# Optimization experiments

Measured on AMD Instinct MI355X. Metric: run time of the kernel, lower is better.

Reference implementation:

```python
import jax, jax.numpy as jnp
import numpy as np

B, D_IN, D_H = 262144, 64, 128


def setup_inputs() -> dict:
    key = jax.random.key(0)
    ks = jax.random.split(key, 15)
    mk = lambda k, shape: jax.random.normal(k, shape, dtype=jnp.float32) * 0.05
    return {
        "x": mk(ks[0], (B, D_IN)),
        "prev_hidden": mk(ks[1], (B, D_H)),
        "prev_memory": mk(ks[2], (B, D_H)),
        "Wi_w": mk(ks[3], (D_H, D_IN)), "Wi_b": mk(ks[4], (D_H,)),
        "Vi_w": mk(ks[5], (D_H, D_H)),  "Vi_b": mk(ks[6], (D_H,)),
        "Wf_w": mk(ks[7], (D_H, D_IN)), "Wf_b": mk(ks[8], (D_H,)),
        "Vf_w": mk(ks[9], (D_H, D_H)),  "Vf_b": mk(ks[10], (D_H,)),
        "Wo_w": mk(ks[11], (D_H, D_IN)), "Wo_b": mk(ks[12], (D_H,)),
        "Vo_w": mk(ks[13], (D_H, D_H)),  "Vo_b": mk(ks[14], (D_H,)),
    }


def _lin(x, w, b):
    # nn.Linear: x @ w.T + b
    return jnp.einsum('bi,oi->bo', x, w) + b


def reference(x, prev_hidden, prev_memory,
              Wi_w, Wi_b, Vi_w, Vi_b,
              Wf_w, Wf_b, Vf_w, Vf_b,
              Wo_w, Wo_b, Vo_w, Vo_b):
    sig = jax.nn.sigmoid
    wi_x = _lin(x, Wi_w, Wi_b)  # reused for both I and C (quirk of source)
    I = sig(wi_x + _lin(prev_hidden, Vi_w, Vi_b))
    F = sig(_lin(x, Wf_w, Wf_b) + _lin(prev_hidden, Vf_w, Vf_b))
    O = sig(_lin(x, Wo_w, Wo_b) + _lin(prev_hidden, Vo_w, Vo_b))
    # source uses Wi/Vi (not Wc/Vc) and sigmoid for the candidate, on F*prev_hidden
    C = sig(wi_x + _lin(F * prev_hidden, Vi_w, Vi_b))
    Ct = F * prev_memory + I * C
    current_hidden = O * jnp.tanh(Ct)
    return (Ct, current_hidden)
```

## Files before the change

### kernel.cpp

```cpp
#include <hip/hip_runtime.h>
#include <hip/hip_bf16.h>

typedef __bf16 bf8 __attribute__((ext_vector_type(8)));
typedef float  f4  __attribute__((ext_vector_type(4)));

#define RT 64
#define MS 4

__device__ __forceinline__ float fsig(float v) {
    return __builtin_amdgcn_rcpf(1.0f + __expf(-v));
}

__device__ __forceinline__ bf8 cvt8(f4 a, f4 b) {
    bf8 r;
    r[0] = (__bf16)a[0]; r[1] = (__bf16)a[1]; r[2] = (__bf16)a[2]; r[3] = (__bf16)a[3];
    r[4] = (__bf16)b[0]; r[5] = (__bf16)b[1]; r[6] = (__bf16)b[2]; r[7] = (__bf16)b[3];
    return r;
}

__device__ __forceinline__ unsigned pk2(float a, float b) {
    union { __bf16 h; unsigned short s; } ua, ub;
    ua.h = (__bf16)a; ub.h = (__bf16)b;
    return ((unsigned)ub.s << 16) | (unsigned)ua.s;
}
__device__ __forceinline__ float upk(unsigned v, int hi) {
    union { unsigned short s; __bf16 h; } u;
    u.s = (unsigned short)(hi ? (v >> 16) : (v & 0xffffu));
    return (float)u.h;
}

__global__ void pack_weights(
    const float* __restrict__ Wi, const float* __restrict__ Vi,
    const float* __restrict__ Wf, const float* __restrict__ Vf,
    const float* __restrict__ Wo, const float* __restrict__ Vo,
    const float* __restrict__ Wib, const float* __restrict__ Vib,
    const float* __restrict__ Wfb, const float* __restrict__ Vfb,
    const float* __restrict__ Wob, const float* __restrict__ Vob,
    __bf16* __restrict__ wsW, float* __restrict__ wsB)
{
    const int t = blockIdx.x * 256 + threadIdx.x;
    if (t < 73728) {
        const int fg   = t >> 9;
        const int l8   = t & 511;
        const int lane = l8 >> 3, j = l8 & 7;
        const int w    = fg / 18, f = fg % 18;
        const int nrow = w * 16 + (lane & 15);
        const int kq   = (lane >> 4) << 3;
        float v;
        if (f < 6) {
            const float* M = (f < 2) ? Wi : (f < 4) ? Wf : Wo;
            v = M[nrow * 64 + (f & 1) * 32 + kq + j];
        } else {
            const int f2 = f - 6;
            const float* M = (f2 < 4) ? Vi : (f2 < 8) ? Vf : Vo;
            v = M[nrow * 128 + (f2 & 3) * 32 + kq + j];
        }
        wsW[t] = (__bf16)v;
    } else if (t < 74112) {
        const int c = t - 73728;
        const int col = c & 127, m = c >> 7;
        wsB[c] = (m == 0) ? Wib[col] + Vib[col]
               : (m == 1) ? Wfb[col] + Vfb[col]
                          : Wob[col] + Vob[col];
    }
}

__global__ __launch_bounds__(512, 2) void lstm_main(
    const float* __restrict__ x, const float* __restrict__ h,
    const float* __restrict__ mem,
    const bf8* __restrict__ wsW, const float* __restrict__ wsB,
    float* __restrict__ out, long long Bn)
{
    __shared__ __align__(16) __bf16 smX[RT * 64];
    __shared__ __align__(16) __bf16 smH[RT * 128];
    __shared__ __align__(16) __bf16 smG[RT * 128 + 64];

    const int tid  = threadIdx.x;
    const int lane = tid & 63;
    const int wv   = tid >> 6;
    const int nrow = wv * 16 + (lane & 15);
    const int kq   = (lane >> 4) << 3;
    const long long b0 = (long long)blockIdx.x * RT;

    const bf8* wbase = wsW + (size_t)wv * 18 * 64 + lane;

    {
        const int rowx = tid >> 3, kbx = tid & 7;
        const float* px = x + (size_t)(b0 + rowx) * 64 + kbx * 8;
        *(bf8*)&smX[rowx * 64 + ((kbx * 8) ^ ((rowx & 7) << 3))] =
            cvt8(*(const f4*)px, *(const f4*)(px + 4));
#pragma unroll
        for (int ph = 0; ph < 2; ++ph) {
            const int task = tid + ph * 512;
            const int rowh = task >> 4, kbh = task & 15;
            const float* q = h + (size_t)(b0 + rowh) * 128 + kbh * 8;
            *(bf8*)&smH[rowh * 128 + ((kbh * 8) ^ ((rowh & 7) << 3))] =
                cvt8(*(const f4*)q, *(const f4*)(q + 4));
        }
    }

    bf8 Wf0 = wbase[2 * 64],  Wf1 = wbase[3 * 64];
    bf8 Vf0 = wbase[10 * 64], Vf1 = wbase[11 * 64];
    bf8 Vf2 = wbase[12 * 64], Vf3 = wbase[13 * 64];
    const float bF = wsB[128 + nrow];
    __syncthreads();

    f4 memv[MS];
#pragma unroll
    for (int ms = 0; ms < MS; ++ms) {
#pragma unroll
        for (int i = 0; i < 4; ++i) {
            const int row = ms * 16 + ((lane >> 4) << 2) + i;
            memv[ms][i] = mem[(size_t)(b0 + row) * 128 + nrow];
        }
    }

    unsigned FP[MS][2];
#pragma unroll
    for (int ms = 0; ms < MS; ++ms) {
        const int rA = ms * 16 + (lane & 15);
        f4 pf = {0.f, 0.f, 0.f, 0.f};
        {
            bf8 a0 = *(const bf8*)&smX[rA * 64 + ((0 * 32 + kq) ^ ((rA & 7) << 3))];
            bf8 a1 = *(const bf8*)&smX[rA * 64 + ((1 * 32 + kq) ^ ((rA & 7) << 3))];
            pf = __builtin_amdgcn_mfma_f32_16x16x32_bf16(a0, Wf0, pf, 0, 0, 0);
            pf = __builtin_amdgcn_mfma_f32_16x16x32_bf16(a1, Wf1, pf, 0, 0, 0);
        }
        {
            bf8 a0 = *(const bf8*)&smH[rA * 128 + ((0 * 32 + kq) ^ ((rA & 7) << 3))];
            bf8 a1 = *(const bf8*)&smH[rA * 128 + ((1 * 32 + kq) ^ ((rA & 7) << 3))];
            bf8 a2 = *(const bf8*)&smH[rA * 128 + ((2 * 32 + kq) ^ ((rA & 7) << 3))];
            bf8 a3 = *(const bf8*)&smH[rA * 128 + ((3 * 32 + kq) ^ ((rA & 7) << 3))];
            pf = __builtin_amdgcn_mfma_f32_16x16x32_bf16(a0, Vf0, pf, 0, 0, 0);
            pf = __builtin_amdgcn_mfma_f32_16x16x32_bf16(a1, Vf1, pf, 0, 0, 0);
            pf = __builtin_amdgcn_mfma_f32_16x16x32_bf16(a2, Vf2, pf, 0, 0, 0);
            pf = __builtin_amdgcn_mfma_f32_16x16x32_bf16(a3, Vf3, pf, 0, 0, 0);
        }
        float fv[4];
#pragma unroll
        for (int i = 0; i < 4; ++i) {
            const float Fi  = fsig(pf[i] + bF);
            const int   row = ms * 16 + ((lane >> 4) << 2) + i;
            const int   e   = row * 128 + (nrow ^ ((row & 7) << 3));
            smG[e] = (__bf16)(Fi * (float)smH[e]);
            fv[i]  = Fi;
        }
        FP[ms][0] = pk2(fv[0], fv[1]);
        FP[ms][1] = pk2(fv[2], fv[3]);
    }
    __syncthreads();
    __builtin_amdgcn_sched_barrier(0);

    bf8 Wi0 = wbase[0],      Wi1 = wbase[64];
    bf8 Vi0 = wbase[6 * 64], Vi1 = wbase[7 * 64];
    bf8 Vi2 = wbase[8 * 64], Vi3 = wbase[9 * 64];
    const float bI = wsB[nrow];
    const size_t outH = (size_t)Bn * 128;

    f4 ThS[MS];
#pragma unroll
    for (int ms = 0; ms < MS; ++ms) {
        const int rA = ms * 16 + (lane & 15);
        f4 wix = {0.f, 0.f, 0.f, 0.f};
        {
            bf8 a0 = *(const bf8*)&smX[rA * 64 + ((0 * 32 + kq) ^ ((rA & 7) << 3))];
            bf8 a1 = *(const bf8*)&smX[rA * 64 + ((1 * 32 + kq) ^ ((rA & 7) << 3))];
            wix = __builtin_amdgcn_mfma_f32_16x16x32_bf16(a0, Wi0, wix, 0, 0, 0);
            wix = __builtin_amdgcn_mfma_f32_16x16x32_bf16(a1, Wi1, wix, 0, 0, 0);
        }
        f4 aI = wix, aC = wix;
        {
            bf8 a0 = *(const bf8*)&smH[rA * 128 + ((0 * 32 + kq) ^ ((rA & 7) << 3))];
            bf8 a1 = *(const bf8*)&smH[rA * 128 + ((1 * 32 + kq) ^ ((rA & 7) << 3))];
            bf8 a2 = *(const bf8*)&smH[rA * 128 + ((2 * 32 + kq) ^ ((rA & 7) << 3))];
            bf8 a3 = *(const bf8*)&smH[rA * 128 + ((3 * 32 + kq) ^ ((rA & 7) << 3))];
            aI = __builtin_amdgcn_mfma_f32_16x16x32_bf16(a0, Vi0, aI, 0, 0, 0);
            aI = __builtin_amdgcn_mfma_f32_16x16x32_bf16(a1, Vi1, aI, 0, 0, 0);
            aI = __builtin_amdgcn_mfma_f32_16x16x32_bf16(a2, Vi2, aI, 0, 0, 0);
            aI = __builtin_amdgcn_mfma_f32_16x16x32_bf16(a3, Vi3, aI, 0, 0, 0);
        }
        {
            bf8 g0 = *(const bf8*)&smG[rA * 128 + ((0 * 32 + kq) ^ ((rA & 7) << 3))];
            bf8 g1 = *(const bf8*)&smG[rA * 128 + ((1 * 32 + kq) ^ ((rA & 7) << 3))];
            bf8 g2 = *(const bf8*)&smG[rA * 128 + ((2 * 32 + kq) ^ ((rA & 7) << 3))];
            bf8 g3 = *(const bf8*)&smG[rA * 128 + ((3 * 32 + kq) ^ ((rA & 7) << 3))];
            aC = __builtin_amdgcn_mfma_f32_16x16x32_bf16(g0, Vi0, aC, 0, 0, 0);
            aC = __builtin_amdgcn_mfma_f32_16x16x32_bf16(g1, Vi1, aC, 0, 0, 0);
            aC = __builtin_amdgcn_mfma_f32_16x16x32_bf16(g2, Vi2, aC, 0, 0, 0);
            aC = __builtin_amdgcn_mfma_f32_16x16x32_bf16(g3, Vi3, aC, 0, 0, 0);
        }
#pragma unroll
        for (int i = 0; i < 4; ++i) {
            const float Iv = fsig(aI[i] + bI);
            const float Cv = fsig(aC[i] + bI);
            const float Fi = upk(FP[ms][i >> 1], i & 1);
            const float ct = Fi * memv[ms][i] + Iv * Cv;
            const float e2 = __expf(2.0f * ct);
            ThS[ms][i] = 1.0f - 2.0f * __builtin_amdgcn_rcpf(e2 + 1.0f);
            const int   row = ms * 16 + ((lane >> 4) << 2) + i;
            const size_t g  = (size_t)(b0 + row) * 128 + nrow;
            out[g] = ct;
        }
    }
    __builtin_amdgcn_sched_barrier(0);

    bf8 Wo0 = wbase[4 * 64],  Wo1 = wbase[5 * 64];
    bf8 Vo0 = wbase[14 * 64], Vo1 = wbase[15 * 64];
    bf8 Vo2 = wbase[16 * 64], Vo3 = wbase[17 * 64];
    const float bO = wsB[256 + nrow];
#pragma unroll
    for (int ms = 0; ms < MS; ++ms) {
        const int rA = ms * 16 + (lane & 15);
        f4 po = {0.f, 0.f, 0.f, 0.f};
        {
            bf8 a0 = *(const bf8*)&smX[rA * 64 + ((0 * 32 + kq) ^ ((rA & 7) << 3))];
            bf8 a1 = *(const bf8*)&smX[rA * 64 + ((1 * 32 + kq) ^ ((rA & 7) << 3))];
            po = __builtin_amdgcn_mfma_f32_16x16x32_bf16(a0, Wo0, po, 0, 0, 0);
            po = __builtin_amdgcn_mfma_f32_16x16x32_bf16(a1, Wo1, po, 0, 0, 0);
        }
        {
            bf8 a0 = *(const bf8*)&smH[rA * 128 + ((0 * 32 + kq) ^ ((rA & 7) << 3))];
            bf8 a1 = *(const bf8*)&smH[rA * 128 + ((1 * 32 + kq) ^ ((rA & 7) << 3))];
            bf8 a2 = *(const bf8*)&smH[rA * 128 + ((2 * 32 + kq) ^ ((rA & 7) << 3))];
            bf8 a3 = *(const bf8*)&smH[rA * 128 + ((3 * 32 + kq) ^ ((rA & 7) << 3))];
            po = __builtin_amdgcn_mfma_f32_16x16x32_bf16(a0, Vo0, po, 0, 0, 0);
            po = __builtin_amdgcn_mfma_f32_16x16x32_bf16(a1, Vo1, po, 0, 0, 0);
            po = __builtin_amdgcn_mfma_f32_16x16x32_bf16(a2, Vo2, po, 0, 0, 0);
            po = __builtin_amdgcn_mfma_f32_16x16x32_bf16(a3, Vo3, po, 0, 0, 0);
        }
#pragma unroll
        for (int i = 0; i < 4; ++i) {
            const float Ov = fsig(po[i] + bO);
            const int   row = ms * 16 + ((lane >> 4) << 2) + i;
            const size_t g  = (size_t)(b0 + row) * 128 + nrow;
            out[outH + g] = Ov * ThS[ms][i];
        }
    }
}

extern "C" void kernel_launch(void* const* d_in, const int* in_sizes, int n_in,
                              void* d_out, int out_size, void* d_ws, size_t ws_size,
                              hipStream_t stream) {
    const float* x   = (const float*)d_in[0];
    const float* h   = (const float*)d_in[1];
    const float* mem = (const float*)d_in[2];
    const float* Wi  = (const float*)d_in[3];
    const float* Wib = (const float*)d_in[4];
    const float* Vi  = (const float*)d_in[5];
    const float* Vib = (const float*)d_in[6];
    const float* Wf  = (const float*)d_in[7];
    const float* Wfb = (const float*)d_in[8];
    const float* Vf  = (const float*)d_in[9];
    const float* Vfb = (const float*)d_in[10];
    const float* Wo  = (const float*)d_in[11];
    const float* Wob = (const float*)d_in[12];
    const float* Vo  = (const float*)d_in[13];
    const float* Vob = (const float*)d_in[14];
    float* out = (float*)d_out;

    __bf16* wsW = (__bf16*)d_ws;
    float*  wsB = (float*)((char*)d_ws + 147456);

    pack_weights<<<290, 256, 0, stream>>>(Wi, Vi, Wf, Vf, Wo, Vo,
                                          Wib, Vib, Wfb, Vfb, Wob, Vob, wsW, wsB);

    const long long Bn = (long long)(in_sizes[1] / 128);
    const int blocks = (int)(Bn / RT);

    lstm_main<<<blocks, 512, 0, stream>>>(x, h, mem, (const bf8*)wsW, wsB, out, Bn);
}
```

Baseline: 160.0 us.

## Double row tile per block, stream memory loads, pack tanh to bf16

Each block now handles 128 rows instead of 64, so per-wave weight fragment loads are amortized over twice as many rows, and the grid is half as large. The up-front load of all prev_memory values into registers is replaced by a rolling three-slot prefetch issued two sub-tiles ahead, and the tanh results held for the output-gate pass are packed to bf16 pairs. Both register changes offset the pressure from the larger tile. LDS use roughly doubles, which may stop two blocks fitting per CU, and storing tanh in bf16 lowers the precision of the hidden-state output.

```diff
diff --git a/kernel.cpp b/kernel.cpp
--- a/kernel.cpp
+++ b/kernel.cpp
@@ -4,8 +4,8 @@
 typedef __bf16 bf8 __attribute__((ext_vector_type(8)));
 typedef float  f4  __attribute__((ext_vector_type(4)));
 
-#define RT 64
-#define MS 4
+#define RT 128
+#define MS 8
 
 __device__ __forceinline__ float fsig(float v) {
     return __builtin_amdgcn_rcpf(1.0f + __expf(-v));
@@ -73,7 +73,7 @@
 {
     __shared__ __align__(16) __bf16 smX[RT * 64];
     __shared__ __align__(16) __bf16 smH[RT * 128];
-    __shared__ __align__(16) __bf16 smG[RT * 128 + 64];
+    __shared__ __align__(16) __bf16 smG[RT * 128];
 
     const int tid  = threadIdx.x;
     const int lane = tid & 63;
@@ -85,12 +85,16 @@
     const bf8* wbase = wsW + (size_t)wv * 18 * 64 + lane;
 
     {
-        const int rowx = tid >> 3, kbx = tid & 7;
-        const float* px = x + (size_t)(b0 + rowx) * 64 + kbx * 8;
-        *(bf8*)&smX[rowx * 64 + ((kbx * 8) ^ ((rowx & 7) << 3))] =
-            cvt8(*(const f4*)px, *(const f4*)(px + 4));
 #pragma unroll
         for (int ph = 0; ph < 2; ++ph) {
+            const int task = tid + ph * 512;
+            const int rowx = task >> 3, kbx = task & 7;
+            const float* px = x + (size_t)(b0 + rowx) * 64 + kbx * 8;
+            *(bf8*)&smX[rowx * 64 + ((kbx * 8) ^ ((rowx & 7) << 3))] =
+                cvt8(*(const f4*)px, *(const f4*)(px + 4));
+        }
+#pragma unroll
+        for (int ph = 0; ph < 4; ++ph) {
             const int task = tid + ph * 512;
             const int rowh = task >> 4, kbh = task & 15;
             const float* q = h + (size_t)(b0 + rowh) * 128 + kbh * 8;
@@ -104,16 +108,6 @@
     bf8 Vf2 = wbase[12 * 64], Vf3 = wbase[13 * 64];
     const float bF = wsB[128 + nrow];
     __syncthreads();
-
-    f4 memv[MS];
-#pragma unroll
-    for (int ms = 0; ms < MS; ++ms) {
-#pragma unroll
-        for (int i = 0; i < 4; ++i) {
-            const int row = ms * 16 + ((lane >> 4) << 2) + i;
-            memv[ms][i] = mem[(size_t)(b0 + row) * 128 + nrow];
-        }
-    }
 
     unsigned FP[MS][2];
 #pragma unroll
@@ -157,9 +151,23 @@
     const float bI = wsB[nrow];
     const size_t outH = (size_t)Bn * 128;
 
-    f4 ThS[MS];
+    auto ldmem = [&](int ms) -> f4 {
+        f4 r;
+#pragma unroll
+        for (int i = 0; i < 4; ++i) {
+            const int row = ms * 16 + ((lane >> 4) << 2) + i;
+            r[i] = mem[(size_t)(b0 + row) * 128 + nrow];
+        }
+        return r;
+    };
+    f4 mv[3];
+    mv[0] = ldmem(0);
+    mv[1] = ldmem(1);
+
+    unsigned ThP[MS][2];
 #pragma unroll
     for (int ms = 0; ms < MS; ++ms) {
+        if (ms + 2 < MS) mv[(ms + 2) % 3] = ldmem(ms + 2);
         const int rA = ms * 16 + (lane & 15);
         f4 wix = {0.f, 0.f, 0.f, 0.f};
         {
@@ -189,18 +197,21 @@
             aC = __builtin_amdgcn_mfma_f32_16x16x32_bf16(g2, Vi2, aC, 0, 0, 0);
             aC = __builtin_amdgcn_mfma_f32_16x16x32_bf16(g3, Vi3, aC, 0, 0, 0);
         }
+        float th[4];
 #pragma unroll
         for (int i = 0; i < 4; ++i) {
             const float Iv = fsig(aI[i] + bI);
             const float Cv = fsig(aC[i] + bI);
             const float Fi = upk(FP[ms][i >> 1], i & 1);
-            const float ct = Fi * memv[ms][i] + Iv * Cv;
+            const float ct = Fi * mv[ms % 3][i] + Iv * Cv;
             const float e2 = __expf(2.0f * ct);
-            ThS[ms][i] = 1.0f - 2.0f * __builtin_amdgcn_rcpf(e2 + 1.0f);
+            th[i] = 1.0f - 2.0f * __builtin_amdgcn_rcpf(e2 + 1.0f);
             const int   row = ms * 16 + ((lane >> 4) << 2) + i;
             const size_t g  = (size_t)(b0 + row) * 128 + nrow;
             out[g] = ct;
         }
+        ThP[ms][0] = pk2(th[0], th[1]);
+        ThP[ms][1] = pk2(th[2], th[3]);
     }
     __builtin_amdgcn_sched_barrier(0);
 
@@ -231,9 +242,10 @@
 #pragma unroll
         for (int i = 0; i < 4; ++i) {
             const float Ov = fsig(po[i] + bO);
+            const float th = upk(ThP[ms][i >> 1], i & 1);
             const int   row = ms * 16 + ((lane >> 4) << 2) + i;
             const size_t g  = (size_t)(b0 + row) * 128 + nrow;
-            out[outH + g] = Ov * ThS[ms][i];
+            out[outH + g] = Ov * th;
         }
     }
 }
```

Result: no change. 158.0 us (-1.2%).

## Make blocks persistent over 8 row tiles with double-buffered x/h prefetch

Applied to the files above, without the earlier changes.

Each block now processes 8 consecutive 64-row tiles instead of one. The x and h loads for the next tile are issued into registers during the current tile's gate computation and written into a second shared-memory buffer at the end of the iteration. The intent is to hide global load latency behind MFMA work and to amortize block launch and bias setup. The tanh values are kept packed as bf16 to limit register pressure. In exchange the grid shrinks 8x, to 512 blocks, which may underfill the CUs, and shared-memory use rises, which can lower occupancy.

```diff
diff --git a/kernel.cpp b/kernel.cpp
--- a/kernel.cpp
+++ b/kernel.cpp
@@ -4,8 +4,9 @@
 typedef __bf16 bf8 __attribute__((ext_vector_type(8)));
 typedef float  f4  __attribute__((ext_vector_type(4)));
 
-#define RT 64
-#define MS 4
+#define RT    64
+#define MS    4
+#define TILES 8
 
 __device__ __forceinline__ float fsig(float v) {
     return __builtin_amdgcn_rcpf(1.0f + __expf(-v));
@@ -71,169 +72,209 @@
     const bf8* __restrict__ wsW, const float* __restrict__ wsB,
     float* __restrict__ out, long long Bn)
 {
-    __shared__ __align__(16) __bf16 smX[RT * 64];
-    __shared__ __align__(16) __bf16 smH[RT * 128];
-    __shared__ __align__(16) __bf16 smG[RT * 128 + 64];
+    __shared__ __align__(16) __bf16 smX[2][RT * 64];
+    __shared__ __align__(16) __bf16 smH[2][RT * 128];
+    __shared__ __align__(16) __bf16 smG[RT * 128];
 
     const int tid  = threadIdx.x;
     const int lane = tid & 63;
     const int wv   = tid >> 6;
     const int nrow = wv * 16 + (lane & 15);
     const int kq   = (lane >> 4) << 3;
-    const long long b0 = (long long)blockIdx.x * RT;
+    const long long tile0 = (long long)blockIdx.x * TILES;
+    const size_t outH = (size_t)Bn * 128;
 
     const bf8* wbase = wsW + (size_t)wv * 18 * 64 + lane;
+    const float bI = wsB[nrow];
+    const float bF = wsB[128 + nrow];
+    const float bO = wsB[256 + nrow];
+
+    const int rowx  = tid >> 3,  kbx  = tid & 7;
+    const int xoff  = rowx * 64 + ((kbx * 8) ^ ((rowx & 7) << 3));
+    const int rowh0 = tid >> 4,  kbh  = tid & 15;
+    const int hoff0 = rowh0 * 128 + ((kbh * 8) ^ ((rowh0 & 7) << 3));
+    const int rowh1 = rowh0 + 32;
+    const int hoff1 = rowh1 * 128 + ((kbh * 8) ^ ((rowh1 & 7) << 3));
 
     {
-        const int rowx = tid >> 3, kbx = tid & 7;
-        const float* px = x + (size_t)(b0 + rowx) * 64 + kbx * 8;
-        *(bf8*)&smX[rowx * 64 + ((kbx * 8) ^ ((rowx & 7) << 3))] =
-            cvt8(*(const f4*)px, *(const f4*)(px + 4));
-#pragma unroll
-        for (int ph = 0; ph < 2; ++ph) {
-            const int task = tid + ph * 512;
-            const int rowh = task >> 4, kbh = task & 15;
-            const float* q = h + (size_t)(b0 + rowh) * 128 + kbh * 8;
-            *(bf8*)&smH[rowh * 128 + ((kbh * 8) ^ ((rowh & 7) << 3))] =
-                cvt8(*(const f4*)q, *(const f4*)(q + 4));
-        }
+        const long long b0s = tile0 * RT;
+        const float* px  = x + (size_t)(b0s + rowx) * 64 + kbx * 8;
+        f4 xa = *(const f4*)px,  xb = *(const f4*)(px + 4);
+        const float* ph0 = h + (size_t)(b0s + rowh0) * 128 + kbh * 8;
+        f4 ha = *(const f4*)ph0, hb = *(const f4*)(ph0 + 4);
+        const float* ph1 = h + (size_t)(b0s + rowh1) * 128 + kbh * 8;
+        f4 hc = *(const f4*)ph1, hd = *(const f4*)(ph1 + 4);
+        *(bf8*)&smX[0][xoff]  = cvt8(xa, xb);
+        *(bf8*)&smH[0][hoff0] = cvt8(ha, hb);
+        *(bf8*)&smH[0][hoff1] = cvt8(hc, hd);
     }
 
-    bf8 Wf0 = wbase[2 * 64],  Wf1 = wbase[3 * 64];
-    bf8 Vf0 = wbase[10 * 64], Vf1 = wbase[11 * 64];
-    bf8 Vf2 = wbase[12 * 64], Vf3 = wbase[13 * 64];
-    const float bF = wsB[128 + nrow];
-    __syncthreads();
-
-    f4 memv[MS];
-#pragma unroll
-    for (int ms = 0; ms < MS; ++ms) {
-#pragma unroll
-        for (int i = 0; i < 4; ++i) {
-            const int row = ms * 16 + ((lane >> 4) << 2) + i;
-            memv[ms][i] = mem[(size_t)(b0 + row) * 128 + nrow];
-        }
-    }
-
-    unsigned FP[MS][2];
-#pragma unroll
-    for (int ms = 0; ms < MS; ++ms) {
-        const int rA = ms * 16 + (lane & 15);
-        f4 pf = {0.f, 0.f, 0.f, 0.f};
-        {
-            bf8 a0 = *(const bf8*)&smX[rA * 64 + ((0 * 32 + kq) ^ ((rA & 7) << 3))];
-            bf8 a1 = *(const bf8*)&smX[rA * 64 + ((1 * 32 + kq) ^ ((rA & 7) << 3))];
-            pf = __builtin_amdgcn_mfma_f32_16x16x32_bf16(a0, Wf0, pf, 0, 0, 0);
-            pf = __builtin_amdgcn_mfma_f32_16x16x32_bf16(a1, Wf1, pf, 0, 0, 0);
-        }
-        {
-            bf8 a0 = *(const bf8*)&smH[rA * 128 + ((0 * 32 + kq) ^ ((rA & 7) << 3))];
-            bf8 a1 = *(const bf8*)&smH[rA * 128 + ((1 * 32 + kq) ^ ((rA & 7) << 3))];
-            bf8 a2 = *(const bf8*)&smH[rA * 128 + ((2 * 32 + kq) ^ ((rA & 7) << 3))];
-            bf8 a3 = *(const bf8*)&smH[rA * 128 + ((3 * 32 + kq) ^ ((rA & 7) << 3))];
-            pf = __builtin_amdgcn_mfma_f32_16x16x32_bf16(a0, Vf0, pf, 0, 0, 0);
-            pf = __builtin_amdgcn_mfma_f32_16x16x32_bf16(a1, Vf1, pf, 0, 0, 0);
-            pf = __builtin_amdgcn_mfma_f32_16x16x32_bf16(a2, Vf2, pf, 0, 0, 0);
-            pf = __builtin_amdgcn_mfma_f32_16x16x32_bf16(a3, Vf3, pf, 0, 0, 0);
-        }
-        float fv[4];
-#pragma unroll
-        for (int i = 0; i < 4; ++i) {
-            const float Fi  = fsig(pf[i] + bF);
-            const int   row = ms * 16 + ((lane >> 4) << 2) + i;
-            const int   e   = row * 128 + (nrow ^ ((row & 7) << 3));
-            smG[e] = (__bf16)(Fi * (float)smH[e]);
-            fv[i]  = Fi;
-        }
-        FP[ms][0] = pk2(fv[0], fv[1]);
-        FP[ms][1] = pk2(fv[2], fv[3]);
-    }
-    __syncthreads();
-    __builtin_amdgcn_sched_barrier(0);
-
-    bf8 Wi0 = wbase[0],      Wi1 = wbase[64];
-    bf8 Vi0 = wbase[6 * 64], Vi1 = wbase[7 * 64];
-    bf8 Vi2 = wbase[8 * 64], Vi3 = wbase[9 * 64];
-    const float bI = wsB[nrow];
-    const size_t outH = (size_t)Bn * 128;
-
-    f4 ThS[MS];
-#pragma unroll
-    for (int ms = 0; ms < MS; ++ms) {
-        const int rA = ms * 16 + (lane & 15);
-        f4 wix = {0.f, 0.f, 0.f, 0.f};
-        {
-            bf8 a0 = *(const bf8*)&smX[rA * 64 + ((0 * 32 + kq) ^ ((rA & 7) << 3))];
-            bf8 a1 = *(const bf8*)&smX[rA * 64 + ((1 * 32 + kq) ^ ((rA & 7) << 3))];
-            wix = __builtin_amdgcn_mfma_f32_16x16x32_bf16(a0, Wi0, wix, 0, 0, 0);
-            wix = __builtin_amdgcn_mfma_f32_16x16x32_bf16(a1, Wi1, wix, 0, 0, 0);
-        }
-        f4 aI = wix, aC = wix;
-        {
-            bf8 a0 = *(const bf8*)&smH[rA * 128 + ((0 * 32 + kq) ^ ((rA & 7) << 3))];
-            bf8 a1 = *(const bf8*)&smH[rA * 128 + ((1 * 32 + kq) ^ ((rA & 7) << 3))];
-            bf8 a2 = *(const bf8*)&smH[rA * 128 + ((2 * 32 + kq) ^ ((rA & 7) << 3))];
-            bf8 a3 = *(const bf8*)&smH[rA * 128 + ((3 * 32 + kq) ^ ((rA & 7) << 3))];
-            aI = __builtin_amdgcn_mfma_f32_16x16x32_bf16(a0, Vi0, aI, 0, 0, 0);
-            aI = __builtin_amdgcn_mfma_f32_16x16x32_bf16(a1, Vi1, aI, 0, 0, 0);
-            aI = __builtin_amdgcn_mfma_f32_16x16x32_bf16(a2, Vi2, aI, 0, 0, 0);
-            aI = __builtin_amdgcn_mfma_f32_16x16x32_bf16(a3, Vi3, aI, 0, 0, 0);
-        }
-        {
-            bf8 g0 = *(const bf8*)&smG[rA * 128 + ((0 * 32 + kq) ^ ((rA & 7) << 3))];
-            bf8 g1 = *(const bf8*)&smG[rA * 128 + ((1 * 32 + kq) ^ ((rA & 7) << 3))];
-            bf8 g2 = *(const bf8*)&smG[rA * 128 + ((2 * 32 + kq) ^ ((rA & 7) << 3))];
-            bf8 g3 = *(const bf8*)&smG[rA * 128 + ((3 * 32 + kq) ^ ((rA & 7) << 3))];
-            aC = __builtin_amdgcn_mfma_f32_16x16x32_bf16(g0, Vi0, aC, 0, 0, 0);
-            aC = __builtin_amdgcn_mfma_f32_16x16x32_bf16(g1, Vi1, aC, 0, 0, 0);
-            aC = __builtin_amdgcn_mfma_f32_16x16x32_bf16(g2, Vi2, aC, 0, 0, 0);
-            aC = __builtin_amdgcn_mfma_f32_16x16x32_bf16(g3, Vi3, aC, 0, 0, 0);
-        }
-#pragma unroll
-        for (int i = 0; i < 4; ++i) {
-            const float Iv = fsig(aI[i] + bI);
-            const float Cv = fsig(aC[i] + bI);
-            const float Fi = upk(FP[ms][i >> 1], i & 1);
-            const float ct = Fi * memv[ms][i] + Iv * Cv;
-            const float e2 = __expf(2.0f * ct);
-            ThS[ms][i] = 1.0f - 2.0f * __builtin_amdgcn_rcpf(e2 + 1.0f);
-            const int   row = ms * 16 + ((lane >> 4) << 2) + i;
-            const size_t g  = (size_t)(b0 + row) * 128 + nrow;
-            out[g] = ct;
-        }
-    }
-    __builtin_amdgcn_sched_barrier(0);
-
-    bf8 Wo0 = wbase[4 * 64],  Wo1 = wbase[5 * 64];
-    bf8 Vo0 = wbase[14 * 64], Vo1 = wbase[15 * 64];
-    bf8 Vo2 = wbase[16 * 64], Vo3 = wbase[17 * 64];
-    const float bO = wsB[256 + nrow];
-#pragma unroll
-    for (int ms = 0; ms < MS; ++ms) {
-        const int rA = ms * 16 + (lane & 15);
-        f4 po = {0.f, 0.f, 0.f, 0.f};
-        {
-            bf8 a0 = *(const bf8*)&smX[rA * 64 + ((0 * 32 + kq) ^ ((rA & 7) << 3))];
-            bf8 a1 = *(const bf8*)&smX[rA * 64 + ((1 * 32 + kq) ^ ((rA & 7) << 3))];
-            po = __builtin_amdgcn_mfma_f32_16x16x32_bf16(a0, Wo0, po, 0, 0, 0);
-            po = __builtin_amdgcn_mfma_f32_16x16x32_bf16(a1, Wo1, po, 0, 0, 0);
-        }
-        {
-            bf8 a0 = *(const bf8*)&smH[rA * 128 + ((0 * 32 + kq) ^ ((rA & 7) << 3))];
-            bf8 a1 = *(const bf8*)&smH[rA * 128 + ((1 * 32 + kq) ^ ((rA & 7) << 3))];
-            bf8 a2 = *(const bf8*)&smH[rA * 128 + ((2 * 32 + kq) ^ ((rA & 7) << 3))];
-            bf8 a3 = *(const bf8*)&smH[rA * 128 + ((3 * 32 + kq) ^ ((rA & 7) << 3))];
-            po = __builtin_amdgcn_mfma_f32_16x16x32_bf16(a0, Vo0, po, 0, 0, 0);
-            po = __builtin_amdgcn_mfma_f32_16x16x32_bf16(a1, Vo1, po, 0, 0, 0);
-            po = __builtin_amdgcn_mfma_f32_16x16x32_bf16(a2, Vo2, po, 0, 0, 0);
-            po = __builtin_amdgcn_mfma_f32_16x16x32_bf16(a3, Vo3, po, 0, 0, 0);
-        }
-#pragma unroll
-        for (int i = 0; i < 4; ++i) {
-            const float Ov = fsig(po[i] + bO);
-            const int   row = ms * 16 + ((lane >> 4) << 2) + i;
-            const size_t g  = (size_t)(b0 + row) * 128 + nrow;
-            out[outH + g] = Ov * ThS[ms][i];
+    for (int t = 0; t < TILES; ++t) {
+        const int  cur = t & 1;
+        const long long b0 = (tile0 + t) * RT;
+        const __bf16* sX = smX[cur];
+        const __bf16* sH = smH[cur];
+        const bool more = (t + 1 < TILES);
+        __syncthreads();
+
+        f4 memv[MS];
+#pragma unroll
+        for (int ms = 0; ms < MS; ++ms) {
+#pragma unroll
+            for (int i = 0; i < 4; ++i) {
+                const int row = ms * 16 + ((lane >> 4) << 2) + i;
+                memv[ms][i] = mem[(size_t)(b0 + row) * 128 + nrow];
+            }
+        }
+
+        bf8 Wf0 = wbase[2 * 64],  Wf1 = wbase[3 * 64];
+        bf8 Vf0 = wbase[10 * 64], Vf1 = wbase[11 * 64];
+        bf8 Vf2 = wbase[12 * 64], Vf3 = wbase[13 * 64];
+        unsigned FP[MS][2];
+#pragma unroll
+        for (int ms = 0; ms < MS; ++ms) {
+            const int rA = ms * 16 + (lane & 15);
+            f4 pf = {0.f, 0.f, 0.f, 0.f};
+            {
+                bf8 a0 = *(const bf8*)&sX[rA * 64 + ((0 * 32 + kq) ^ ((rA & 7) << 3))];
+                bf8 a1 = *(const bf8*)&sX[rA * 64 + ((1 * 32 + kq) ^ ((rA & 7) << 3))];
+                pf = __builtin_amdgcn_mfma_f32_16x16x32_bf16(a0, Wf0, pf, 0, 0, 0);
+                pf = __builtin_amdgcn_mfma_f32_16x16x32_bf16(a1, Wf1, pf, 0, 0, 0);
+            }
+            {
+                bf8 a0 = *(const bf8*)&sH[rA * 128 + ((0 * 32 + kq) ^ ((rA & 7) << 3))];
+                bf8 a1 = *(const bf8*)&sH[rA * 128 + ((1 * 32 + kq) ^ ((rA & 7) << 3))];
+                bf8 a2 = *(const bf8*)&sH[rA * 128 + ((2 * 32 + kq) ^ ((rA & 7) << 3))];
+                bf8 a3 = *(const bf8*)&sH[rA * 128 + ((3 * 32 + kq) ^ ((rA & 7) << 3))];
+                pf = __builtin_amdgcn_mfma_f32_16x16x32_bf16(a0, Vf0, pf, 0, 0, 0);
+                pf = __builtin_amdgcn_mfma_f32_16x16x32_bf16(a1, Vf1, pf, 0, 0, 0);
+                pf = __builtin_amdgcn_mfma_f32_16x16x32_bf16(a2, Vf2, pf, 0, 0, 0);
+                pf = __builtin_amdgcn_mfma_f32_16x16x32_bf16(a3, Vf3, pf, 0, 0, 0);
+            }
+            float fv[4];
+#pragma unroll
+            for (int i = 0; i < 4; ++i) {
+                const float Fi  = fsig(pf[i] + bF);
+                const int   row = ms * 16 + ((lane >> 4) << 2) + i;
+                const int   e   = row * 128 + (nrow ^ ((row & 7) << 3));
+                smG[e] = (__bf16)(Fi * (float)sH[e]);
+                fv[i]  = Fi;
+            }
+            FP[ms][0] = pk2(fv[0], fv[1]);
+            FP[ms][1] = pk2(fv[2], fv[3]);
+        }
+        __syncthreads();
+        __builtin_amdgcn_sched_barrier(0);
+
+        f4 ha, hb, hc, hd;
+        if (more) {
+            const long long b1 = b0 + RT;
+            const float* ph0 = h + (size_t)(b1 + rowh0) * 128 + kbh * 8;
+            ha = *(const f4*)ph0; hb = *(const f4*)(ph0 + 4);
+            const float* ph1 = h + (size_t)(b1 + rowh1) * 128 + kbh * 8;
+            hc = *(const f4*)ph1; hd = *(const f4*)(ph1 + 4);
+        }
+        __builtin_amdgcn_sched_barrier(0);
+
+        bf8 Wi0 = wbase[0],      Wi1 = wbase[64];
+        bf8 Vi0 = wbase[6 * 64], Vi1 = wbase[7 * 64];
+        bf8 Vi2 = wbase[8 * 64], Vi3 = wbase[9 * 64];
+        unsigned ThP[MS][2];
+#pragma unroll
+        for (int ms = 0; ms < MS; ++ms) {
+            const int rA = ms * 16 + (lane & 15);
+            f4 wix = {0.f, 0.f, 0.f, 0.f};
+            {
+                bf8 a0 = *(const bf8*)&sX[rA * 64 + ((0 * 32 + kq) ^ ((rA & 7) << 3))];
+                bf8 a1 = *(const bf8*)&sX[rA * 64 + ((1 * 32 + kq) ^ ((rA & 7) << 3))];
+                wix = __builtin_amdgcn_mfma_f32_16x16x32_bf16(a0, Wi0, wix, 0, 0, 0);
+                wix = __builtin_amdgcn_mfma_f32_16x16x32_bf16(a1, Wi1, wix, 0, 0, 0);
+            }
+            f4 aI = wix, aC = wix;
+            {
+                bf8 a0 = *(const bf8*)&sH[rA * 128 + ((0 * 32 + kq) ^ ((rA & 7) << 3))];
+                bf8 a1 = *(const bf8*)&sH[rA * 128 + ((1 * 32 + kq) ^ ((rA & 7) << 3))];
+                bf8 a2 = *(const bf8*)&sH[rA * 128 + ((2 * 32 + kq) ^ ((rA & 7) << 3))];
+                bf8 a3 = *(const bf8*)&sH[rA * 128 + ((3 * 32 + kq) ^ ((rA & 7) << 3))];
+                aI = __builtin_amdgcn_mfma_f32_16x16x32_bf16(a0, Vi0, aI, 0, 0, 0);
+                aI = __builtin_amdgcn_mfma_f32_16x16x32_bf16(a1, Vi1, aI, 0, 0, 0);
+                aI = __builtin_amdgcn_mfma_f32_16x16x32_bf16(a2, Vi2, aI, 0, 0, 0);
+                aI = __builtin_amdgcn_mfma_f32_16x16x32_bf16(a3, Vi3, aI, 0, 0, 0);
+            }
+            {
+                bf8 g0 = *(const bf8*)&smG[rA * 128 + ((0 * 32 + kq) ^ ((rA & 7) << 3))];
+                bf8 g1 = *(const bf8*)&smG[rA * 128 + ((1 * 32 + kq) ^ ((rA & 7) << 3))];
+                bf8 g2 = *(const bf8*)&smG[rA * 128 + ((2 * 32 + kq) ^ ((rA & 7) << 3))];
+                bf8 g3 = *(const bf8*)&smG[rA * 128 + ((3 * 32 + kq) ^ ((rA & 7) << 3))];
+                aC = __builtin_amdgcn_mfma_f32_16x16x32_bf16(g0, Vi0, aC, 0, 0, 0);
+                aC = __builtin_amdgcn_mfma_f32_16x16x32_bf16(g1, Vi1, aC, 0, 0, 0);
+                aC = __builtin_amdgcn_mfma_f32_16x16x32_bf16(g2, Vi2, aC, 0, 0, 0);
+                aC = __builtin_amdgcn_mfma_f32_16x16x32_bf16(g3, Vi3, aC, 0, 0, 0);
+            }
+            float th[4];
+#pragma unroll
+            for (int i = 0; i < 4; ++i) {
+                const float Iv = fsig(aI[i] + bI);
+                const float Cv = fsig(aC[i] + bI);
+                const float Fi = upk(FP[ms][i >> 1], i & 1);
+                const float ct = Fi * memv[ms][i] + Iv * Cv;
+                const float e2 = __expf(2.0f * ct);
+                th[i] = 1.0f - 2.0f * __builtin_amdgcn_rcpf(e2 + 1.0f);
+                const int   row = ms * 16 + ((lane >> 4) << 2) + i;
+                const size_t g  = (size_t)(b0 + row) * 128 + nrow;
+                out[g] = ct;
+            }
+            ThP[ms][0] = pk2(th[0], th[1]);
+            ThP[ms][1] = pk2(th[2], th[3]);
+        }
+        __builtin_amdgcn_sched_barrier(0);
+
+        f4 xa, xb;
+        if (more) {
+            const float* px = x + (size_t)(b0 + RT + rowx) * 64 + kbx * 8;
+            xa = *(const f4*)px; xb = *(const f4*)(px + 4);
+        }
+        __builtin_amdgcn_sched_barrier(0);
+
+        bf8 Wo0 = wbase[4 * 64],  Wo1 = wbase[5 * 64];
+        bf8 Vo0 = wbase[14 * 64], Vo1 = wbase[15 * 64];
+        bf8 Vo2 = wbase[16 * 64], Vo3 = wbase[17 * 64];
+#pragma unroll
+        for (int ms = 0; ms < MS; ++ms) {
+            const int rA = ms * 16 + (lane & 15);
+            f4 po = {0.f, 0.f, 0.f, 0.f};
+            {
+                bf8 a0 = *(const bf8*)&sX[rA * 64 + ((0 * 32 + kq) ^ ((rA & 7) << 3))];
+                bf8 a1 = *(const bf8*)&sX[rA * 64 + ((1 * 32 + kq) ^ ((rA & 7) << 3))];
+                po = __builtin_amdgcn_mfma_f32_16x16x32_bf16(a0, Wo0, po, 0, 0, 0);
+                po = __builtin_amdgcn_mfma_f32_16x16x32_bf16(a1, Wo1, po, 0, 0, 0);
+            }
+            {
+                bf8 a0 = *(const bf8*)&sH[rA * 128 + ((0 * 32 + kq) ^ ((rA & 7) << 3))];
+                bf8 a1 = *(const bf8*)&sH[rA * 128 + ((1 * 32 + kq) ^ ((rA & 7) << 3))];
+                bf8 a2 = *(const bf8*)&sH[rA * 128 + ((2 * 32 + kq) ^ ((rA & 7) << 3))];
+                bf8 a3 = *(const bf8*)&sH[rA * 128 + ((3 * 32 + kq) ^ ((rA & 7) << 3))];
+                po = __builtin_amdgcn_mfma_f32_16x16x32_bf16(a0, Vo0, po, 0, 0, 0);
+                po = __builtin_amdgcn_mfma_f32_16x16x32_bf16(a1, Vo1, po, 0, 0, 0);
+                po = __builtin_amdgcn_mfma_f32_16x16x32_bf16(a2, Vo2, po, 0, 0, 0);
+                po = __builtin_amdgcn_mfma_f32_16x16x32_bf16(a3, Vo3, po, 0, 0, 0);
+            }
+#pragma unroll
+            for (int i = 0; i < 4; ++i) {
+                const float Ov = fsig(po[i] + bO);
+                const float th = upk(ThP[ms][i >> 1], i & 1);
+                const int   row = ms * 16 + ((lane >> 4) << 2) + i;
+                const size_t g  = (size_t)(b0 + row) * 128 + nrow;
+                out[outH + g] = Ov * th;
+            }
+        }
+
+        if (more) {
+            __bf16* dX = smX[cur ^ 1];
+            __bf16* dH = smH[cur ^ 1];
+            *(bf8*)&dX[xoff]  = cvt8(xa, xb);
+            *(bf8*)&dH[hoff0] = cvt8(ha, hb);
+            *(bf8*)&dH[hoff1] = cvt8(hc, hd);
         }
     }
 }
@@ -265,7 +306,7 @@
                                           Wib, Vib, Wfb, Vfb, Wob, Vob, wsW, wsB);
 
     const long long Bn = (long long)(in_sizes[1] / 128);
-    const int blocks = (int)(Bn / RT);
+    const int blocks = (int)(Bn / (RT * TILES));
 
     lstm_main<<<blocks, 512, 0, stream>>>(x, h, mem, (const bf8*)wsW, wsB, out, Bn);
 }
```

New measurement: 169.4 us. 1.06x slower.
